# Optimization experiments

Hardware: AMD Instinct MI355X
Metric: run time of the kernel (lower is better)

## Reference

```python
import jax, jax.numpy as jnp
import numpy as np

CE_SLICES = [(1,10),(12,29),(30,33),(33,40),(40,64),(64,79),(79,84),(84,94),(94,96),(96,99),(99,105),(105,113),(116,122),(122,128),(128,151),(151,159),(160,165)]
MSE_COLS = [0,10,11,29,113,114,115,159,165,166,167]
BINS = 800
RATIO_JSD = 0.1  # stand-in for par.RATIO_JSD (not defined in source)
B = 262144


def setup_inputs() -> dict:
    key = jax.random.key(0)
    k1, k2, k3, k4 = jax.random.split(key, 4)
    data_encoded = jax.random.normal(k1, (B, 11), dtype=jnp.float32)
    data_decoded = jax.random.normal(k2, (B, 168), dtype=jnp.float32)
    data_true = jax.random.normal(k3, (B, 168), dtype=jnp.float32)
    # categorical blocks of data_true must be one-hot (nonzero-based decode)
    for j, (s, e) in enumerate(CE_SLICES):
        lab = jax.random.randint(jax.random.fold_in(k3, j), (B,), 0, e - s)
        data_true = data_true.at[:, s:e].set(jax.nn.one_hot(lab, e - s, dtype=jnp.float32))
    label_true = jax.random.randint(k4, (B, 1), 0, 2).astype(jnp.float32)
    return {"data_encoded": data_encoded, "data_decoded": data_decoded,
            "data_true": data_true, "label_true": label_true, "batch_size": B}


def _ce(logits, labels):
    # F.cross_entropy with mean reduction
    logp = jax.nn.log_softmax(logits, axis=-1)
    return -jnp.mean(jnp.take_along_axis(logp, labels[:, None], axis=1))


def _hist(x, mn, mx, mask):
    # torch.histc semantics: BINS equal bins on [mn, mx], top edge inclusive.
    t = (x - mn) / (mx - mn)
    idx = jnp.clip(jnp.floor(t * BINS).astype(jnp.int32), 0, BINS - 1)
    return jax.ops.segment_sum(mask, idx, num_segments=BINS)


def _kl(p, q, eps=1e-12):
    return jnp.sum(jnp.where(p > 0, p * jnp.log((p + eps) / (q + eps)), 0.0))


def reference(data_encoded, data_decoded, data_true, label_true, batch_size):
    # ---- MSE losses over 11 scalar columns (vectorized) ----
    cols = jnp.array(MSE_COLS)
    diff = data_decoded[:, cols] - data_true[:, cols]            # [B, 11]
    mse_loss = jnp.sum(jnp.mean(diff * diff, axis=0))

    # ---- 17 cross-entropy heads (labels decoded from one-hot blocks) ----
    ce_loss = jnp.float32(0.0)
    for s, e in CE_SLICES:
        labels = jnp.argmax(data_true[:, s:e], axis=1)           # == first nonzero for one-hot
        ce_loss = ce_loss + _ce(data_decoded[:, s:e], labels)

    # ---- JSD between male/female histograms of first 10 encoded dims ----
    combined = jnp.concatenate([data_encoded, label_true], axis=1)  # [B, 12]
    mn = jnp.min(combined, axis=0)
    mx = jnp.max(combined, axis=0)
    male = (combined[:, 11] == 0).astype(jnp.float32)
    female = (combined[:, 11] == 1).astype(jnp.float32)
    cols10 = combined[:, :10].T                                  # [10, B]
    hist = jax.vmap(_hist, in_axes=(0, 0, 0, None))              # [10, BINS]
    m_h = hist(cols10, mn[:10], mx[:10], male) / jnp.sum(male)
    f_h = hist(cols10, mn[:10], mx[:10], female) / jnp.sum(female)
    mid = 0.5 * (m_h + f_h)
    kld = 0.5 * (_kl(m_h, mid) + _kl(f_h, mid))                  # Jensen-Shannon divergence

    multi = (1.0 - RATIO_JSD) * (mse_loss + ce_loss) + RATIO_JSD * kld
    return jnp.stack([multi, mse_loss, ce_loss, RATIO_JSD * kld])
```

## Files before the change

### kernel.cpp

```cpp
#include <hip/hip_runtime.h>
#include <math.h>


#define BINS 800
#define NHCOLS 10
#define HB 64

#define MIN_OFF 0
#define MAX_OFF 16
#define CNT_OFF 32
#define SUM_OFF 34
#define MH_OFF  64
#define FH_OFF  8064
#define PART_OFF 16384
#define WS_INIT_U32 64

__device__ __forceinline__ unsigned f2ord(float f) {
  unsigned u = __float_as_uint(f);
  return (u & 0x80000000u) ? ~u : (u | 0x80000000u);
}
__device__ __forceinline__ float ord2f(unsigned e) {
  return __uint_as_float((e & 0x80000000u) ? (e & 0x7FFFFFFFu) : ~e);
}

__global__ void k_init(unsigned* __restrict__ ws) {
  int i = blockIdx.x * blockDim.x + threadIdx.x;
  if (i < WS_INIT_U32) ws[i] = (i < 11) ? 0xFFFFFFFFu : 0u;
}

__global__ __launch_bounds__(256) void k_minmax(const float* __restrict__ enc,
                                                const float* __restrict__ lab,
                                                unsigned* __restrict__ ws, int B) {
  const int tid    = blockIdx.x * blockDim.x + threadIdx.x;
  const int stride = gridDim.x * blockDim.x;
  const int c      = tid % 11;
  unsigned mn = 0xFFFFFFFFu, mx = 0u;
  const long long total = (long long)B * 11;
  for (long long i = tid; i < total; i += stride) {
    unsigned e = f2ord(enc[i]);
    mn = mn < e ? mn : e;
    mx = mx > e ? mx : e;
  }
  __shared__ unsigned smn[11], smx[11], scnt[2];
  if (threadIdx.x < 11) { smn[threadIdx.x] = 0xFFFFFFFFu; smx[threadIdx.x] = 0u; }
  if (threadIdx.x < 2)  scnt[threadIdx.x] = 0u;
  __syncthreads();
  atomicMin(&smn[c], mn);
  atomicMax(&smx[c], mx);
  unsigned m = 0, f = 0;
  for (int i = tid; i < B; i += stride) {
    float v = lab[i];
    m += (v == 0.0f);
    f += (v == 1.0f);
  }
  atomicAdd(&scnt[0], m);
  atomicAdd(&scnt[1], f);
  __syncthreads();
  if (threadIdx.x < 11) {
    atomicMin(&ws[MIN_OFF + threadIdx.x], smn[threadIdx.x]);
    atomicMax(&ws[MAX_OFF + threadIdx.x], smx[threadIdx.x]);
  }
  if (threadIdx.x == 11) atomicAdd(&ws[CNT_OFF + 0], scnt[0]);
  if (threadIdx.x == 12) atomicAdd(&ws[CNT_OFF + 1], scnt[1]);
}

__global__ __launch_bounds__(256) void k_hist(const float* __restrict__ enc,
                                              const float* __restrict__ lab,
                                              unsigned* __restrict__ ws, int B) {
  __shared__ unsigned h[2][NHCOLS * BINS];
  unsigned* hf = &h[0][0];
  for (int i = threadIdx.x; i < 2 * NHCOLS * BINS; i += blockDim.x) hf[i] = 0u;
  float mn[NHCOLS], rng[NHCOLS];
#pragma unroll
  for (int c = 0; c < NHCOLS; ++c) {
    float lo = ord2f(ws[MIN_OFF + c]);
    float hi = ord2f(ws[MAX_OFF + c]);
    mn[c] = lo; rng[c] = hi - lo;
  }
  __syncthreads();
  const int sub = (threadIdx.x >> 6) & 1;
  for (int r = blockIdx.x * 256 + threadIdx.x; r < B; r += HB * 256) {
    float lv = lab[r];
    unsigned add = (lv == 0.0f) ? 1u : ((lv == 1.0f) ? 0x10000u : 0u);
    if (add) {
      const float* row = enc + (long long)r * 11;
#pragma unroll
      for (int c = 0; c < NHCOLS; ++c) {
        float t = (row[c] - mn[c]) / rng[c];
        int b = (int)floorf(t * 800.0f);
        b = b < 0 ? 0 : (b > BINS - 1 ? BINS - 1 : b);
        atomicAdd(&h[sub][c * BINS + b], add);
      }
    }
  }
  __syncthreads();
  for (int i = threadIdx.x; i < NHCOLS * BINS; i += blockDim.x)
    ws[PART_OFF + blockIdx.x * (NHCOLS * BINS) + i] = h[0][i] + h[1][i];
}

__global__ __launch_bounds__(256) void k_merge(unsigned* __restrict__ ws) {
  int i = blockIdx.x * blockDim.x + threadIdx.x;
  if (i >= NHCOLS * BINS) return;
  unsigned m = 0, f = 0;
  for (int p = 0; p < HB; ++p) {
    unsigned v = ws[PART_OFF + p * (NHCOLS * BINS) + i];
    m += v & 0xFFFFu;
    f += v >> 16;
  }
  ws[MH_OFF + i] = m;
  ws[FH_OFF + i] = f;
}

__host__ __device__ constexpr int slice_of(int c) {
  return (c>=1&&c<10)?0:(c>=12&&c<29)?1:(c>=30&&c<33)?2:(c>=33&&c<40)?3:
         (c>=40&&c<64)?4:(c>=64&&c<79)?5:(c>=79&&c<84)?6:(c>=84&&c<94)?7:
         (c>=94&&c<96)?8:(c>=96&&c<99)?9:(c>=99&&c<105)?10:(c>=105&&c<113)?11:
         (c>=116&&c<122)?12:(c>=122&&c<128)?13:(c>=128&&c<151)?14:
         (c>=151&&c<159)?15:(c>=160&&c<165)?16:-1;
}
__host__ __device__ constexpr bool mse_of(int c) {
  return c==0||c==10||c==11||c==29||c==113||c==114||c==115||c==159||
         c==165||c==166||c==167;
}

template<int I, int K>
__device__ __forceinline__ void elem(const float (&d)[11][4], const float (&t)[11][4],
                                     float (&s)[17], float &dot, float &mse, int j) {
  constexpr int c0 = 16*I + K, c1 = c0+4, c2 = c0+8, c3 = c0+12;
  constexpr int cem = ((c0<168 && slice_of(c0)>=0)?1:0) |
                      ((c1<168 && slice_of(c1)>=0)?2:0) |
                      ((c2<168 && slice_of(c2)>=0)?4:0) |
                      ((c3<168 && slice_of(c3)>=0)?8:0);
  constexpr int msm = ((c0<168 && mse_of(c0))?1:0) | ((c1<168 && mse_of(c1))?2:0) |
                      ((c2<168 && mse_of(c2))?4:0) | ((c3<168 && mse_of(c3))?8:0);
  const float dv = d[I][K], tv = t[I][K];
  if constexpr (cem != 0) {
    float e = __expf(dv);
    if constexpr (cem & 1) s[slice_of(c0)] += (j == 0) ? e : 0.0f;
    if constexpr (cem & 2) s[slice_of(c1)] += (j == 1) ? e : 0.0f;
    if constexpr (cem & 4) s[slice_of(c2)] += (j == 2) ? e : 0.0f;
    if constexpr (cem & 8) s[slice_of(c3)] += (j == 3) ? e : 0.0f;
    dot += ((cem >> j) & 1) ? tv * dv : 0.0f;
  }
  if constexpr (msm != 0) {
    float df = dv - tv;
    mse += ((msm >> j) & 1) ? df * df : 0.0f;
  }
}

template<int I>
__device__ __forceinline__ void elem_row(const float (&d)[11][4], const float (&t)[11][4],
                                         float (&s)[17], float &dot, float &mse, int j) {
  elem<I,0>(d, t, s, dot, mse, j);
  elem<I,1>(d, t, s, dot, mse, j);
  elem<I,2>(d, t, s, dot, mse, j);
  elem<I,3>(d, t, s, dot, mse, j);
}

__global__ __launch_bounds__(256) void k_main(const float* __restrict__ dec,
                                              const float* __restrict__ tru,
                                              float* __restrict__ wsf, int B) {
  const int lane = threadIdx.x & 63;
  const int wid  = threadIdx.x >> 6;
  const int j    = lane & 3;
  const int row  = blockIdx.x * 64 + (wid << 4) + (lane >> 2);
  const bool valid = row < B;

  float d[11][4], t[11][4];
  const float4* d4 = (const float4*)(dec + (size_t)row * 168);
  const float4* t4 = (const float4*)(tru + (size_t)row * 168);
#pragma unroll
  for (int i = 0; i < 11; ++i) {
    const int w = 4 * i + j;
    float4 dv = make_float4(0.f, 0.f, 0.f, 0.f);
    float4 tv = make_float4(0.f, 0.f, 0.f, 0.f);
    if (valid && w < 42) { dv = d4[w]; tv = t4[w]; }
    d[i][0] = dv.x; d[i][1] = dv.y; d[i][2] = dv.z; d[i][3] = dv.w;
    t[i][0] = tv.x; t[i][1] = tv.y; t[i][2] = tv.z; t[i][3] = tv.w;
  }

  float s[17];
#pragma unroll
  for (int k = 0; k < 17; ++k) s[k] = 0.0f;
  float dot = 0.0f, mse = 0.0f;

  elem_row<0>(d, t, s, dot, mse, j);
  elem_row<1>(d, t, s, dot, mse, j);
  elem_row<2>(d, t, s, dot, mse, j);
  elem_row<3>(d, t, s, dot, mse, j);
  elem_row<4>(d, t, s, dot, mse, j);
  elem_row<5>(d, t, s, dot, mse, j);
  elem_row<6>(d, t, s, dot, mse, j);
  elem_row<7>(d, t, s, dot, mse, j);
  elem_row<8>(d, t, s, dot, mse, j);
  elem_row<9>(d, t, s, dot, mse, j);
  elem_row<10>(d, t, s, dot, mse, j);

  dot += __shfl_xor(dot, 1, 64);
  dot += __shfl_xor(dot, 2, 64);
#pragma unroll
  for (int k = 0; k < 17; ++k) {
    s[k] += __shfl_xor(s[k], 1, 64);
    s[k] += __shfl_xor(s[k], 2, 64);
  }
  float ce = -dot;
#pragma unroll
  for (int k = 0; k < 17; ++k) ce += __logf(s[k]);

  ce  = (valid && j == 0) ? ce : 0.0f;
  mse = valid ? mse : 0.0f;

  __shared__ float sm[4], sc[4];
#pragma unroll
  for (int off = 32; off > 0; off >>= 1) {
    mse += __shfl_down(mse, off, 64);
    ce  += __shfl_down(ce, off, 64);
  }
  if (lane == 0) { sm[wid] = mse; sc[wid] = ce; }
  __syncthreads();
  if (threadIdx.x == 0) {
    atomicAdd(&wsf[SUM_OFF + 0], sm[0] + sm[1] + sm[2] + sm[3]);
    atomicAdd(&wsf[SUM_OFF + 1], sc[0] + sc[1] + sc[2] + sc[3]);
  }
}

__global__ __launch_bounds__(256) void k_final(const unsigned* __restrict__ ws,
                                               float* __restrict__ out, int B) {
  const float* wsf = (const float*)ws;
  float male   = (float)ws[CNT_OFF + 0];
  float female = (float)ws[CNT_OFF + 1];
  float local = 0.0f;
  for (int i = threadIdx.x; i < NHCOLS * BINS; i += blockDim.x) {
    float mh  = (float)ws[MH_OFF + i] / male;
    float fh  = (float)ws[FH_OFF + i] / female;
    float mid = 0.5f * (mh + fh);
    if (mh > 0.0f) local += mh * logf((mh + 1e-12f) / (mid + 1e-12f));
    if (fh > 0.0f) local += fh * logf((fh + 1e-12f) / (mid + 1e-12f));
  }
  __shared__ float s[4];
  int lane = threadIdx.x & 63, wid = threadIdx.x >> 6;
#pragma unroll
  for (int off = 32; off > 0; off >>= 1) local += __shfl_down(local, off, 64);
  if (lane == 0) s[wid] = local;
  __syncthreads();
  if (threadIdx.x == 0) {
    float kld   = 0.5f * (s[0] + s[1] + s[2] + s[3]);
    float mse   = wsf[SUM_OFF + 0] / (float)B;
    float ce    = wsf[SUM_OFF + 1] / (float)B;
    float multi = 0.9f * (mse + ce) + 0.1f * kld;
    out[0] = multi;
    out[1] = mse;
    out[2] = ce;
    out[3] = 0.1f * kld;
  }
}

extern "C" void kernel_launch(void* const* d_in, const int* in_sizes, int n_in,
                              void* d_out, int out_size, void* d_ws, size_t ws_size,
                              hipStream_t stream) {
  (void)n_in; (void)out_size; (void)ws_size;
  const float* enc = (const float*)d_in[0];
  const float* dec = (const float*)d_in[1];
  const float* tru = (const float*)d_in[2];
  const float* lab = (const float*)d_in[3];
  const int B = in_sizes[3];
  unsigned* ws = (unsigned*)d_ws;
  float* out = (float*)d_out;

  hipLaunchKernelGGL(k_init, dim3(1), dim3(64), 0, stream, ws);
  hipLaunchKernelGGL(k_minmax, dim3(352), dim3(256), 0, stream, enc, lab, ws, B);
  hipLaunchKernelGGL(k_hist, dim3(HB), dim3(256), 0, stream, enc, lab, ws, B);
  hipLaunchKernelGGL(k_merge, dim3((NHCOLS * BINS + 255) / 256), dim3(256), 0, stream, ws);
  hipLaunchKernelGGL(k_main, dim3((B + 63) / 64), dim3(256), 0, stream,
                     dec, tru, (float*)ws, B);
  hipLaunchKernelGGL(k_final, dim3(1), dim3(256), 0, stream, ws, out, B);
}
```

Measured before the change: 446.1 us.

## Widen histogram grid with coalesced element-wise indexing and unpredicated main loads

The histogram kernel now launches up to 512 blocks instead of 64, sized to the available workspace. Each thread walks flat enc elements rather than whole rows, so global reads coalesce, and min/range now come from shared memory. The merge kernel loops over the runtime block count, so it reads more partial histograms. The main kernel clamps row and column indices to make loads unconditional, adds a scheduling barrier after the loads and sets a two-blocks-per-CU launch bound, which may raise register pressure or spill.

```diff
diff --git a/kernel.cpp b/kernel.cpp
--- a/kernel.cpp
+++ b/kernel.cpp
@@ -4,7 +4,7 @@
 
 #define BINS 800
 #define NHCOLS 10
-#define HB 64
+#define HB_MAX 512
 
 #define MIN_OFF 0
 #define MAX_OFF 16
@@ -66,27 +66,29 @@
 
 __global__ __launch_bounds__(256) void k_hist(const float* __restrict__ enc,
                                               const float* __restrict__ lab,
-                                              unsigned* __restrict__ ws, int B) {
+                                              unsigned* __restrict__ ws, int B, int hb) {
   __shared__ unsigned h[2][NHCOLS * BINS];
+  __shared__ float smn[NHCOLS], srng[NHCOLS];
   unsigned* hf = &h[0][0];
   for (int i = threadIdx.x; i < 2 * NHCOLS * BINS; i += blockDim.x) hf[i] = 0u;
-  float mn[NHCOLS], rng[NHCOLS];
-#pragma unroll
-  for (int c = 0; c < NHCOLS; ++c) {
-    float lo = ord2f(ws[MIN_OFF + c]);
-    float hi = ord2f(ws[MAX_OFF + c]);
-    mn[c] = lo; rng[c] = hi - lo;
+  if (threadIdx.x < NHCOLS) {
+    float lo = ord2f(ws[MIN_OFF + threadIdx.x]);
+    float hi = ord2f(ws[MAX_OFF + threadIdx.x]);
+    smn[threadIdx.x] = lo;
+    srng[threadIdx.x] = hi - lo;
   }
   __syncthreads();
   const int sub = (threadIdx.x >> 6) & 1;
-  for (int r = blockIdx.x * 256 + threadIdx.x; r < B; r += HB * 256) {
-    float lv = lab[r];
-    unsigned add = (lv == 0.0f) ? 1u : ((lv == 1.0f) ? 0x10000u : 0u);
-    if (add) {
-      const float* row = enc + (long long)r * 11;
-#pragma unroll
-      for (int c = 0; c < NHCOLS; ++c) {
-        float t = (row[c] - mn[c]) / rng[c];
+  const int total  = B * 11;
+  const int stride = hb << 8;
+  for (int i = (blockIdx.x << 8) + threadIdx.x; i < total; i += stride) {
+    const int r = i / 11;
+    const int c = i - r * 11;
+    if (c < NHCOLS) {
+      float lv = lab[r];
+      unsigned add = (lv == 0.0f) ? 1u : ((lv == 1.0f) ? 0x10000u : 0u);
+      if (add) {
+        float t = (enc[i] - smn[c]) / srng[c];
         int b = (int)floorf(t * 800.0f);
         b = b < 0 ? 0 : (b > BINS - 1 ? BINS - 1 : b);
         atomicAdd(&h[sub][c * BINS + b], add);
@@ -95,15 +97,16 @@
   }
   __syncthreads();
   for (int i = threadIdx.x; i < NHCOLS * BINS; i += blockDim.x)
-    ws[PART_OFF + blockIdx.x * (NHCOLS * BINS) + i] = h[0][i] + h[1][i];
-}
-
-__global__ __launch_bounds__(256) void k_merge(unsigned* __restrict__ ws) {
+    ws[PART_OFF + (size_t)blockIdx.x * (NHCOLS * BINS) + i] = h[0][i] + h[1][i];
+}
+
+__global__ __launch_bounds__(256) void k_merge(unsigned* __restrict__ ws, int hb) {
   int i = blockIdx.x * blockDim.x + threadIdx.x;
   if (i >= NHCOLS * BINS) return;
   unsigned m = 0, f = 0;
-  for (int p = 0; p < HB; ++p) {
-    unsigned v = ws[PART_OFF + p * (NHCOLS * BINS) + i];
+  const unsigned* p = ws + PART_OFF + i;
+  for (int q = 0; q < hb; ++q) {
+    unsigned v = p[(size_t)q * (NHCOLS * BINS)];
     m += v & 0xFFFFu;
     f += v >> 16;
   }
@@ -157,27 +160,29 @@
   elem<I,3>(d, t, s, dot, mse, j);
 }
 
-__global__ __launch_bounds__(256) void k_main(const float* __restrict__ dec,
-                                              const float* __restrict__ tru,
-                                              float* __restrict__ wsf, int B) {
+__global__ __launch_bounds__(256, 2) void k_main(const float* __restrict__ dec,
+                                                 const float* __restrict__ tru,
+                                                 float* __restrict__ wsf, int B) {
   const int lane = threadIdx.x & 63;
   const int wid  = threadIdx.x >> 6;
   const int j    = lane & 3;
   const int row  = blockIdx.x * 64 + (wid << 4) + (lane >> 2);
   const bool valid = row < B;
+  const int rowc = valid ? row : (B - 1);
 
   float d[11][4], t[11][4];
-  const float4* d4 = (const float4*)(dec + (size_t)row * 168);
-  const float4* t4 = (const float4*)(tru + (size_t)row * 168);
+  const float4* d4 = (const float4*)(dec + (size_t)rowc * 168);
+  const float4* t4 = (const float4*)(tru + (size_t)rowc * 168);
 #pragma unroll
   for (int i = 0; i < 11; ++i) {
-    const int w = 4 * i + j;
-    float4 dv = make_float4(0.f, 0.f, 0.f, 0.f);
-    float4 tv = make_float4(0.f, 0.f, 0.f, 0.f);
-    if (valid && w < 42) { dv = d4[w]; tv = t4[w]; }
+    int w = 4 * i + j;
+    w = w > 41 ? 41 : w;
+    const float4 dv = d4[w];
+    const float4 tv = t4[w];
     d[i][0] = dv.x; d[i][1] = dv.y; d[i][2] = dv.z; d[i][3] = dv.w;
     t[i][0] = tv.x; t[i][1] = tv.y; t[i][2] = tv.z; t[i][3] = tv.w;
   }
+  __builtin_amdgcn_sched_barrier(0);
 
   float s[17];
 #pragma unroll
@@ -258,7 +263,7 @@
 extern "C" void kernel_launch(void* const* d_in, const int* in_sizes, int n_in,
                               void* d_out, int out_size, void* d_ws, size_t ws_size,
                               hipStream_t stream) {
-  (void)n_in; (void)out_size; (void)ws_size;
+  (void)n_in; (void)out_size;
   const float* enc = (const float*)d_in[0];
   const float* dec = (const float*)d_in[1];
   const float* tru = (const float*)d_in[2];
@@ -267,10 +272,22 @@
   unsigned* ws = (unsigned*)d_ws;
   float* out = (float*)d_out;
 
+  int hb = HB_MAX;
+  {
+    size_t avail = ws_size / 4;
+    if (avail > (size_t)PART_OFF) {
+      size_t cap = (avail - (size_t)PART_OFF) / (size_t)(NHCOLS * BINS);
+      if ((size_t)hb > cap) hb = (int)cap;
+    } else {
+      hb = 1;
+    }
+    if (hb < 1) hb = 1;
+  }
+
   hipLaunchKernelGGL(k_init, dim3(1), dim3(64), 0, stream, ws);
   hipLaunchKernelGGL(k_minmax, dim3(352), dim3(256), 0, stream, enc, lab, ws, B);
-  hipLaunchKernelGGL(k_hist, dim3(HB), dim3(256), 0, stream, enc, lab, ws, B);
-  hipLaunchKernelGGL(k_merge, dim3((NHCOLS * BINS + 255) / 256), dim3(256), 0, stream, ws);
+  hipLaunchKernelGGL(k_hist, dim3(hb), dim3(256), 0, stream, enc, lab, ws, B, hb);
+  hipLaunchKernelGGL(k_merge, dim3((NHCOLS * BINS + 255) / 256), dim3(256), 0, stream, ws, hb);
   hipLaunchKernelGGL(k_main, dim3((B + 63) / 64), dim3(256), 0, stream,
                      dec, tru, (float*)ws, B);
   hipLaunchKernelGGL(k_final, dim3(1), dim3(256), 0, stream, ws, out, B);
```

Measured after the change: 514.0 us. +15.2%, slower.
